# Kernel optimization log

Hardware: AMD Instinct MI355X
Metric: run time of the kernel (lower is better)

## Reference

```python
import jax, jax.numpy as jnp
import numpy as np


def setup_inputs() -> dict:
    key = jax.random.key(0)
    ks = jax.random.split(key, 7)
    Bsz, Dm, L, N = 2, 1536, 2048, 16
    x = jax.random.normal(ks[0], (Bsz, Dm, L), jnp.float32)
    delta = jax.random.uniform(ks[1], (Bsz, Dm, L), jnp.float32, 1e-3, 0.1)  # positive step sizes
    A = -jax.random.uniform(ks[2], (Dm, N), jnp.float32, 0.5, 1.5)  # negative real A for stability
    B = jax.random.normal(ks[3], (Bsz, N, L), jnp.float32)
    C = jax.random.normal(ks[4], (Bsz, N, L), jnp.float32)
    D = jax.random.normal(ks[5], (Dm,), jnp.float32)
    z = jax.random.normal(ks[6], (Bsz, Dm, L), jnp.float32)
    return {"x": x, "delta": delta, "A": A, "B": B, "C": C, "D": D, "z": z}


def reference(x, delta, A, B, C, D, z):
    # x, delta, z: [b, d, l]; A: [d, n]; B, C: [b, n, l]; D: [d]
    dtype_in = x.dtype
    x = x.astype(jnp.float32)
    delta = delta.astype(jnp.float32)
    Bm = B.astype(jnp.float32)
    Cm = C.astype(jnp.float32)

    # time-major for scan: [l, b, ...]
    dl = jnp.moveaxis(delta, 2, 0)   # l b d
    xl = jnp.moveaxis(x, 2, 0)       # l b d
    Bl = jnp.moveaxis(Bm, 2, 0)      # l b n
    Cl = jnp.moveaxis(Cm, 2, 0)      # l b n

    h0 = jnp.zeros((x.shape[0], A.shape[0], A.shape[1]), jnp.float32)  # b d n

    def step(h, inp):
        d_t, x_t, B_t, C_t = inp
        deltaA = jnp.exp(d_t[:, :, None] * A[None, :, :])      # exp(einsum('bdl,dn->bdln')) at token t
        deltaB = d_t[:, :, None] * B_t[:, None, :]              # einsum('bdl,bnl->bdln') at token t
        h = deltaA * h + deltaB * x_t[:, :, None]               # Hx update
        y = jnp.einsum('bdn,bn->bd', h, C_t)                    # Yh readout
        return h, y

    _, ys = jax.lax.scan(step, h0, (dl, xl, Bl, Cl))            # ys: [l, b, d]
    y = jnp.moveaxis(ys, 0, 2)                                  # b d l

    out = y + x * D[None, :, None]
    out = out * jax.nn.silu(z)
    return out.astype(dtype_in)
```

## Files before the change

### kernel.cpp

```cpp
#include <hip/hip_runtime.h>
#include <hip/hip_fp16.h>

#define LOG2E 1.44269504088896340736f
#define DM 1536
#define LL  2048
#define NN  16
#define NCH 64
#define CL  32

__device__ __forceinline__ float fexp2(float v){ return __builtin_amdgcn_exp2f(v); }
__device__ __forceinline__ float frcp(float v){ return __builtin_amdgcn_rcpf(v); }

__device__ __forceinline__ void load16(const float* __restrict__ p, float* v){
    const float4 a=*(const float4*)p,     b=*(const float4*)(p+4),
                 c=*(const float4*)(p+8), d=*(const float4*)(p+12);
    v[0]=a.x; v[1]=a.y; v[2]=a.z; v[3]=a.w;
    v[4]=b.x; v[5]=b.y; v[6]=b.z; v[7]=b.w;
    v[8]=c.x; v[9]=c.y; v[10]=c.z; v[11]=c.w;
    v[12]=d.x; v[13]=d.y; v[14]=d.z; v[15]=d.w;
}

__device__ __forceinline__ float packdx(float d, float x){
    unsigned u = (unsigned)__half_as_ushort(__float2half_rn(d))
               | ((unsigned)__half_as_ushort(__float2half_rn(x)) << 16);
    return __uint_as_float(u);
}
__device__ __forceinline__ void unpackdx(float f, float& d, float& x){
    const unsigned u = __float_as_uint(f);
    d = __half2float(__ushort_as_half((unsigned short)(u & 0xffffu)));
    x = __half2float(__ushort_as_half((unsigned short)(u >> 16)));
}

__global__ __launch_bounds__(256) void transpose_bc(
        const float* __restrict__ Bm, const float* __restrict__ Cm,
        float* __restrict__ Bt, float* __restrict__ Ct){
    const int q  = blockIdx.x*256 + threadIdx.x;
    const int t0 = (q & 511) << 2;
    const int n  = (q >> 9) & 15;
    const int b  = q >> 13;
    const long i = (long)(b*NN + n)*LL + t0;
    const float4 bv = *(const float4*)(Bm + i);
    const float4 cv = *(const float4*)(Cm + i);
    const float bb[4]={bv.x,bv.y,bv.z,bv.w}, cc[4]={cv.x,cv.y,cv.z,cv.w};
#pragma unroll
    for (int j=0;j<4;++j){
        const int t = t0 + j;
        const int o = ((b*CL + (t&31))*NCH + (t>>5))*NN + n;
        Bt[o] = bb[j];
        Ct[o] = cc[j];
    }
}

__global__ __launch_bounds__(256, 3) void ssm_scan(
    const float* __restrict__ x, const float* __restrict__ delta,
    const float* __restrict__ A, const float* __restrict__ Dv,
    const float* __restrict__ z, const float* __restrict__ Bt,
    const float* __restrict__ Ct, float* __restrict__ out)
{
    __shared__ float sdx[4][CL*64];

    const int lane = threadIdx.x & 63;
    const int w    = threadIdx.x >> 6;
    const int row  = blockIdx.x*4 + w;
    const int b    = (row >= DM) ? 1 : 0;
    const int d    = row - b*DM;
    float* sw = sdx[w];

    const long base = (long)row*LL;
    const float* gd = delta + base;
    const float* gx = x + base;

    for (int k=0;k<LL;k+=256){
        const int t0 = k + lane*4;
        const float4 dv = *(const float4*)(gd + t0);
        const float4 xv = *(const float4*)(gx + t0);
        const float dd[4]={dv.x,dv.y,dv.z,dv.w};
        const float xx[4]={xv.x,xv.y,xv.z,xv.w};
#pragma unroll
        for (int j=0;j<4;++j){
            const int t = t0 + j, r = t & 31, c = t >> 5;
            sw[r*64 + (c^r)] = packdx(dd[j], xx[j]);
        }
    }

    float A2[NN];
#pragma unroll
    for (int n=0;n<NN;++n) A2[n] = A[d*NN+n] * LOG2E;

    const float* bq = Bt + (long)b*(CL*NCH*NN) + lane*NN;
    const float* cq = Ct + (long)b*(CL*NCH*NN) + lane*NN;

    float G[NN];
#pragma unroll
    for (int n=0;n<NN;++n) G[n] = 0.f;
    float dsum = 0.f;
    float bb[NN];
    load16(bq, bb);
#pragma unroll 2
    for (int r=0;r<CL;++r){
        float nb[NN];
        if (r+1 < CL) load16(bq + (r+1)*(NCH*NN), nb);
        float d_r, x_r;
        unpackdx(sw[r*64 + (lane^r)], d_r, x_r);
        dsum += d_r;
        const float dx = d_r * x_r;
#pragma unroll
        for (int n=0;n<NN;++n){
            const float e = fexp2(d_r*A2[n]);
            G[n] = __builtin_fmaf(e, G[n], bb[n]*dx);
        }
        if (r+1 < CL){
#pragma unroll
            for (int n=0;n<NN;++n) bb[n] = nb[n];
        }
    }
    float P[NN];
#pragma unroll
    for (int n=0;n<NN;++n) P[n] = fexp2(dsum*A2[n]);

#pragma unroll
    for (int s=1;s<64;s<<=1){
#pragma unroll
        for (int n=0;n<NN;++n){
            const float pl = __shfl_up(P[n], s);
            const float gl = __shfl_up(G[n], s);
            if (lane >= s){
                G[n] = __builtin_fmaf(P[n], gl, G[n]);
                P[n] *= pl;
            }
        }
    }
    float h[NN];
#pragma unroll
    for (int n=0;n<NN;++n){
        const float gp = __shfl_up(G[n], 1);
        h[n] = (lane==0) ? 0.f : gp;
    }

    const float Dd = Dv[d];
    float cc[NN];
    load16(bq, bb);
    load16(cq, cc);
#pragma unroll 2
    for (int r=0;r<CL;++r){
        float nb[NN], nc[NN];
        if (r+1 < CL){
            load16(bq + (r+1)*(NCH*NN), nb);
            load16(cq + (r+1)*(NCH*NN), nc);
        }
        const int a = r*64 + (lane ^ r);
        float d_r, x_r;
        unpackdx(sw[a], d_r, x_r);
        const float dx = d_r * x_r;
        float y0=0.f, y1=0.f, y2=0.f, y3=0.f;
#pragma unroll
        for (int n=0;n<NN;n+=4){
            const float e0=fexp2(d_r*A2[n+0]);
            h[n+0]=__builtin_fmaf(e0,h[n+0],bb[n+0]*dx); y0=__builtin_fmaf(h[n+0],cc[n+0],y0);
            const float e1=fexp2(d_r*A2[n+1]);
            h[n+1]=__builtin_fmaf(e1,h[n+1],bb[n+1]*dx); y1=__builtin_fmaf(h[n+1],cc[n+1],y1);
            const float e2=fexp2(d_r*A2[n+2]);
            h[n+2]=__builtin_fmaf(e2,h[n+2],bb[n+2]*dx); y2=__builtin_fmaf(h[n+2],cc[n+2],y2);
            const float e3=fexp2(d_r*A2[n+3]);
            h[n+3]=__builtin_fmaf(e3,h[n+3],bb[n+3]*dx); y3=__builtin_fmaf(h[n+3],cc[n+3],y3);
        }
        const float y = (y0+y1)+(y2+y3);
        sw[a] = __builtin_fmaf(x_r, Dd, y);
        if (r+1 < CL){
#pragma unroll
            for (int n=0;n<NN;++n){ bb[n]=nb[n]; cc[n]=nc[n]; }
        }
    }

    const float* gz = z + base;
    float* go = out + base;
    for (int k=0;k<LL;k+=256){
        const int t0 = k + lane*4;
        const float4 zv = *(const float4*)(gz + t0);
        const float zz[4]={zv.x,zv.y,zv.z,zv.w};
        float o[4];
#pragma unroll
        for (int j=0;j<4;++j){
            const int t = t0 + j, r = t & 31, c = t >> 5;
            const float yd = sw[r*64 + (c^r)];
            const float sig = frcp(1.f + fexp2(-zz[j]*LOG2E));
            o[j] = yd * (zz[j]*sig);
        }
        float4 o4 = {o[0],o[1],o[2],o[3]};
        *(float4*)(go + t0) = o4;
    }
}

extern "C" void kernel_launch(void* const* d_in, const int* in_sizes, int n_in,
                              void* d_out, int out_size, void* d_ws, size_t ws_size,
                              hipStream_t stream) {
    const float* x     = (const float*)d_in[0];
    const float* delta = (const float*)d_in[1];
    const float* A     = (const float*)d_in[2];
    const float* B     = (const float*)d_in[3];
    const float* C     = (const float*)d_in[4];
    const float* Dv    = (const float*)d_in[5];
    const float* z     = (const float*)d_in[6];
    float* out = (float*)d_out;

    float* Bt = (float*)d_ws;
    float* Ct = Bt + 2*LL*NN;

    transpose_bc<<<dim3(64), dim3(256), 0, stream>>>(B, C, Bt, Ct);
    ssm_scan<<<dim3((2*DM)/4), dim3(256), 0, stream>>>(x, delta, A, Dv, z, Bt, Ct, out);
}
```

Baseline: 185.2 us.

## Process two channels per wavefront and store B/C interleaved in fp16

Each wavefront now scans two d-channels instead of one, so every B/C load serves two channels. B and C are converted to fp16 and interleaved into one 64-byte record per timestep and chunk, which halves their bandwidth and removes the explicit prefetch double-buffering. Blocks shrink to 128 threads with shared memory holding float2 pairs. The trade-offs are higher register pressure from the duplicated 16-element state arrays (launch bounds 128,2) and extra fp16 rounding of B and C.

```diff
diff --git a/kernel.cpp b/kernel.cpp
--- a/kernel.cpp
+++ b/kernel.cpp
@@ -11,15 +11,6 @@
 __device__ __forceinline__ float fexp2(float v){ return __builtin_amdgcn_exp2f(v); }
 __device__ __forceinline__ float frcp(float v){ return __builtin_amdgcn_rcpf(v); }
 
-__device__ __forceinline__ void load16(const float* __restrict__ p, float* v){
-    const float4 a=*(const float4*)p,     b=*(const float4*)(p+4),
-                 c=*(const float4*)(p+8), d=*(const float4*)(p+12);
-    v[0]=a.x; v[1]=a.y; v[2]=a.z; v[3]=a.w;
-    v[4]=b.x; v[5]=b.y; v[6]=b.z; v[7]=b.w;
-    v[8]=c.x; v[9]=c.y; v[10]=c.z; v[11]=c.w;
-    v[12]=d.x; v[13]=d.y; v[14]=d.z; v[15]=d.w;
-}
-
 __device__ __forceinline__ float packdx(float d, float x){
     unsigned u = (unsigned)__half_as_ushort(__float2half_rn(d))
                | ((unsigned)__half_as_ushort(__float2half_rn(x)) << 16);
@@ -30,10 +21,22 @@
     d = __half2float(__ushort_as_half((unsigned short)(u & 0xffffu)));
     x = __half2float(__ushort_as_half((unsigned short)(u >> 16)));
 }
+__device__ __forceinline__ void unpack8(const float4 f, float* o){
+    const unsigned u0=__float_as_uint(f.x), u1=__float_as_uint(f.y),
+                   u2=__float_as_uint(f.z), u3=__float_as_uint(f.w);
+    o[0]=__half2float(__ushort_as_half((unsigned short)(u0&0xffffu)));
+    o[1]=__half2float(__ushort_as_half((unsigned short)(u0>>16)));
+    o[2]=__half2float(__ushort_as_half((unsigned short)(u1&0xffffu)));
+    o[3]=__half2float(__ushort_as_half((unsigned short)(u1>>16)));
+    o[4]=__half2float(__ushort_as_half((unsigned short)(u2&0xffffu)));
+    o[5]=__half2float(__ushort_as_half((unsigned short)(u2>>16)));
+    o[6]=__half2float(__ushort_as_half((unsigned short)(u3&0xffffu)));
+    o[7]=__half2float(__ushort_as_half((unsigned short)(u3>>16)));
+}
 
 __global__ __launch_bounds__(256) void transpose_bc(
         const float* __restrict__ Bm, const float* __restrict__ Cm,
-        float* __restrict__ Bt, float* __restrict__ Ct){
+        __half* __restrict__ BC){
     const int q  = blockIdx.x*256 + threadIdx.x;
     const int t0 = (q & 511) << 2;
     const int n  = (q >> 9) & 15;
@@ -45,149 +48,156 @@
 #pragma unroll
     for (int j=0;j<4;++j){
         const int t = t0 + j;
-        const int o = ((b*CL + (t&31))*NCH + (t>>5))*NN + n;
-        Bt[o] = bb[j];
-        Ct[o] = cc[j];
-    }
-}
-
-__global__ __launch_bounds__(256, 3) void ssm_scan(
+        const long o = ((long)((b*CL + (t&31))*NCH + (t>>5)))*32 + n;
+        BC[o]      = __float2half_rn(bb[j]);
+        BC[o + 16] = __float2half_rn(cc[j]);
+    }
+}
+
+__global__ __launch_bounds__(128, 2) void ssm_scan(
     const float* __restrict__ x, const float* __restrict__ delta,
     const float* __restrict__ A, const float* __restrict__ Dv,
-    const float* __restrict__ z, const float* __restrict__ Bt,
-    const float* __restrict__ Ct, float* __restrict__ out)
+    const float* __restrict__ z, const __half* __restrict__ BC,
+    float* __restrict__ out)
 {
-    __shared__ float sdx[4][CL*64];
+    __shared__ float2 sdx[2][CL*64];
 
     const int lane = threadIdx.x & 63;
     const int w    = threadIdx.x >> 6;
-    const int row  = blockIdx.x*4 + w;
-    const int b    = (row >= DM) ? 1 : 0;
-    const int d    = row - b*DM;
-    float* sw = sdx[w];
-
-    const long base = (long)row*LL;
-    const float* gd = delta + base;
-    const float* gx = x + base;
+    const int row0 = blockIdx.x*4 + w*2;
+    const int b    = (row0 >= DM) ? 1 : 0;
+    const int d0   = row0 - b*DM;
+    float2* sw = sdx[w];
+
+    const long base0 = (long)row0*LL;
+    const long base1 = base0 + LL;
+    const float* gd0 = delta + base0; const float* gx0 = x + base0;
+    const float* gd1 = delta + base1; const float* gx1 = x + base1;
 
     for (int k=0;k<LL;k+=256){
         const int t0 = k + lane*4;
-        const float4 dv = *(const float4*)(gd + t0);
-        const float4 xv = *(const float4*)(gx + t0);
-        const float dd[4]={dv.x,dv.y,dv.z,dv.w};
-        const float xx[4]={xv.x,xv.y,xv.z,xv.w};
+        const float4 dv0 = *(const float4*)(gd0 + t0);
+        const float4 xv0 = *(const float4*)(gx0 + t0);
+        const float4 dv1 = *(const float4*)(gd1 + t0);
+        const float4 xv1 = *(const float4*)(gx1 + t0);
+        const float dd0[4]={dv0.x,dv0.y,dv0.z,dv0.w}, xx0[4]={xv0.x,xv0.y,xv0.z,xv0.w};
+        const float dd1[4]={dv1.x,dv1.y,dv1.z,dv1.w}, xx1[4]={xv1.x,xv1.y,xv1.z,xv1.w};
 #pragma unroll
         for (int j=0;j<4;++j){
             const int t = t0 + j, r = t & 31, c = t >> 5;
-            sw[r*64 + (c^r)] = packdx(dd[j], xx[j]);
-        }
-    }
-
-    float A2[NN];
-#pragma unroll
-    for (int n=0;n<NN;++n) A2[n] = A[d*NN+n] * LOG2E;
-
-    const float* bq = Bt + (long)b*(CL*NCH*NN) + lane*NN;
-    const float* cq = Ct + (long)b*(CL*NCH*NN) + lane*NN;
-
-    float G[NN];
-#pragma unroll
-    for (int n=0;n<NN;++n) G[n] = 0.f;
-    float dsum = 0.f;
-    float bb[NN];
-    load16(bq, bb);
+            float2 wd; wd.x = packdx(dd0[j], xx0[j]); wd.y = packdx(dd1[j], xx1[j]);
+            sw[r*64 + (c^r)] = wd;
+        }
+    }
+
+    float A20[NN], A21[NN];
+#pragma unroll
+    for (int n=0;n<NN;++n){
+        A20[n] = A[d0*NN+n]     * LOG2E;
+        A21[n] = A[(d0+1)*NN+n] * LOG2E;
+    }
+
+    const __half* bc = BC + (long)b*65536 + lane*32;
+
+    float G0[NN], G1[NN];
+#pragma unroll
+    for (int n=0;n<NN;++n){ G0[n]=0.f; G1[n]=0.f; }
+    float ds0=0.f, ds1=0.f;
 #pragma unroll 2
     for (int r=0;r<CL;++r){
-        float nb[NN];
-        if (r+1 < CL) load16(bq + (r+1)*(NCH*NN), nb);
-        float d_r, x_r;
-        unpackdx(sw[r*64 + (lane^r)], d_r, x_r);
-        dsum += d_r;
-        const float dx = d_r * x_r;
+        const float2 wd = sw[r*64 + (lane^r)];
+        const float4* rec = (const float4*)(bc + (long)r*2048);
+        float bb[16];
+        unpack8(rec[0], bb); unpack8(rec[1], bb+8);
+        float d_0,x_0,d_1,x_1;
+        unpackdx(wd.x, d_0, x_0); unpackdx(wd.y, d_1, x_1);
+        ds0 += d_0; ds1 += d_1;
+        const float dx0 = d_0*x_0, dx1 = d_1*x_1;
 #pragma unroll
         for (int n=0;n<NN;++n){
-            const float e = fexp2(d_r*A2[n]);
-            G[n] = __builtin_fmaf(e, G[n], bb[n]*dx);
-        }
-        if (r+1 < CL){
-#pragma unroll
-            for (int n=0;n<NN;++n) bb[n] = nb[n];
-        }
-    }
-    float P[NN];
-#pragma unroll
-    for (int n=0;n<NN;++n) P[n] = fexp2(dsum*A2[n]);
-
-#pragma unroll
-    for (int s=1;s<64;s<<=1){
+            const float e0 = fexp2(d_0*A20[n]);
+            G0[n] = __builtin_fmaf(e0, G0[n], bb[n]*dx0);
+            const float e1 = fexp2(d_1*A21[n]);
+            G1[n] = __builtin_fmaf(e1, G1[n], bb[n]*dx1);
+        }
+    }
+
+    float h0[NN], h1[NN];
+    {
+        float P0[NN], P1[NN];
+#pragma unroll
+        for (int n=0;n<NN;++n){ P0[n]=fexp2(ds0*A20[n]); P1[n]=fexp2(ds1*A21[n]); }
+#pragma unroll
+        for (int s=1;s<64;s<<=1){
+#pragma unroll
+            for (int n=0;n<NN;++n){
+                const float pl0=__shfl_up(P0[n],s), gl0=__shfl_up(G0[n],s);
+                const float pl1=__shfl_up(P1[n],s), gl1=__shfl_up(G1[n],s);
+                if (lane >= s){
+                    G0[n]=__builtin_fmaf(P0[n],gl0,G0[n]); P0[n]*=pl0;
+                    G1[n]=__builtin_fmaf(P1[n],gl1,G1[n]); P1[n]*=pl1;
+                }
+            }
+        }
 #pragma unroll
         for (int n=0;n<NN;++n){
-            const float pl = __shfl_up(P[n], s);
-            const float gl = __shfl_up(G[n], s);
-            if (lane >= s){
-                G[n] = __builtin_fmaf(P[n], gl, G[n]);
-                P[n] *= pl;
-            }
-        }
-    }
-    float h[NN];
-#pragma unroll
-    for (int n=0;n<NN;++n){
-        const float gp = __shfl_up(G[n], 1);
-        h[n] = (lane==0) ? 0.f : gp;
-    }
-
-    const float Dd = Dv[d];
-    float cc[NN];
-    load16(bq, bb);
-    load16(cq, cc);
+            const float g0=__shfl_up(G0[n],1), g1=__shfl_up(G1[n],1);
+            h0[n] = (lane==0)?0.f:g0;
+            h1[n] = (lane==0)?0.f:g1;
+        }
+    }
+
+    const float Dd0 = Dv[d0], Dd1 = Dv[d0+1];
 #pragma unroll 2
     for (int r=0;r<CL;++r){
-        float nb[NN], nc[NN];
-        if (r+1 < CL){
-            load16(bq + (r+1)*(NCH*NN), nb);
-            load16(cq + (r+1)*(NCH*NN), nc);
-        }
-        const int a = r*64 + (lane ^ r);
-        float d_r, x_r;
-        unpackdx(sw[a], d_r, x_r);
-        const float dx = d_r * x_r;
-        float y0=0.f, y1=0.f, y2=0.f, y3=0.f;
-#pragma unroll
-        for (int n=0;n<NN;n+=4){
-            const float e0=fexp2(d_r*A2[n+0]);
-            h[n+0]=__builtin_fmaf(e0,h[n+0],bb[n+0]*dx); y0=__builtin_fmaf(h[n+0],cc[n+0],y0);
-            const float e1=fexp2(d_r*A2[n+1]);
-            h[n+1]=__builtin_fmaf(e1,h[n+1],bb[n+1]*dx); y1=__builtin_fmaf(h[n+1],cc[n+1],y1);
-            const float e2=fexp2(d_r*A2[n+2]);
-            h[n+2]=__builtin_fmaf(e2,h[n+2],bb[n+2]*dx); y2=__builtin_fmaf(h[n+2],cc[n+2],y2);
-            const float e3=fexp2(d_r*A2[n+3]);
-            h[n+3]=__builtin_fmaf(e3,h[n+3],bb[n+3]*dx); y3=__builtin_fmaf(h[n+3],cc[n+3],y3);
-        }
-        const float y = (y0+y1)+(y2+y3);
-        sw[a] = __builtin_fmaf(x_r, Dd, y);
-        if (r+1 < CL){
-#pragma unroll
-            for (int n=0;n<NN;++n){ bb[n]=nb[n]; cc[n]=nc[n]; }
-        }
-    }
-
-    const float* gz = z + base;
-    float* go = out + base;
+        const int slot = r*64 + (lane^r);
+        const float2 wd = sw[slot];
+        const float4* rec = (const float4*)(bc + (long)r*2048);
+        float bb[16], cc[16];
+        unpack8(rec[0], bb); unpack8(rec[1], bb+8);
+        unpack8(rec[2], cc); unpack8(rec[3], cc+8);
+        float d_0,x_0,d_1,x_1;
+        unpackdx(wd.x, d_0, x_0); unpackdx(wd.y, d_1, x_1);
+        const float dx0 = d_0*x_0, dx1 = d_1*x_1;
+        float ya0=0.f, yb0=0.f, ya1=0.f, yb1=0.f;
+#pragma unroll
+        for (int n=0;n<NN;n+=2){
+            const float e0a = fexp2(d_0*A20[n]);
+            h0[n]  =__builtin_fmaf(e0a,h0[n],  bb[n]*dx0);   ya0=__builtin_fmaf(h0[n],  cc[n],  ya0);
+            const float e0b = fexp2(d_0*A20[n+1]);
+            h0[n+1]=__builtin_fmaf(e0b,h0[n+1],bb[n+1]*dx0); yb0=__builtin_fmaf(h0[n+1],cc[n+1],yb0);
+            const float e1a = fexp2(d_1*A21[n]);
+            h1[n]  =__builtin_fmaf(e1a,h1[n],  bb[n]*dx1);   ya1=__builtin_fmaf(h1[n],  cc[n],  ya1);
+            const float e1b = fexp2(d_1*A21[n+1]);
+            h1[n+1]=__builtin_fmaf(e1b,h1[n+1],bb[n+1]*dx1); yb1=__builtin_fmaf(h1[n+1],cc[n+1],yb1);
+        }
+        float2 yo;
+        yo.x = __builtin_fmaf(x_0, Dd0, ya0+yb0);
+        yo.y = __builtin_fmaf(x_1, Dd1, ya1+yb1);
+        sw[slot] = yo;
+    }
+
+    const float* gz0 = z + base0; const float* gz1 = z + base1;
+    float* go0 = out + base0;     float* go1 = out + base1;
     for (int k=0;k<LL;k+=256){
         const int t0 = k + lane*4;
-        const float4 zv = *(const float4*)(gz + t0);
-        const float zz[4]={zv.x,zv.y,zv.z,zv.w};
-        float o[4];
+        const float4 zv0 = *(const float4*)(gz0 + t0);
+        const float4 zv1 = *(const float4*)(gz1 + t0);
+        const float zz0[4]={zv0.x,zv0.y,zv0.z,zv0.w}, zz1[4]={zv1.x,zv1.y,zv1.z,zv1.w};
+        float o0[4], o1[4];
 #pragma unroll
         for (int j=0;j<4;++j){
             const int t = t0 + j, r = t & 31, c = t >> 5;
-            const float yd = sw[r*64 + (c^r)];
-            const float sig = frcp(1.f + fexp2(-zz[j]*LOG2E));
-            o[j] = yd * (zz[j]*sig);
-        }
-        float4 o4 = {o[0],o[1],o[2],o[3]};
-        *(float4*)(go + t0) = o4;
+            const float2 wd = sw[r*64 + (c^r)];
+            const float s0 = frcp(1.f + fexp2(-zz0[j]*LOG2E));
+            const float s1 = frcp(1.f + fexp2(-zz1[j]*LOG2E));
+            o0[j] = wd.x * (zz0[j]*s0);
+            o1[j] = wd.y * (zz1[j]*s1);
+        }
+        float4 a = {o0[0],o0[1],o0[2],o0[3]};
+        float4 bq = {o1[0],o1[1],o1[2],o1[3]};
+        *(float4*)(go0 + t0) = a;
+        *(float4*)(go1 + t0) = bq;
     }
 }
 
@@ -203,9 +213,8 @@
     const float* z     = (const float*)d_in[6];
     float* out = (float*)d_out;
 
-    float* Bt = (float*)d_ws;
-    float* Ct = Bt + 2*LL*NN;
-
-    transpose_bc<<<dim3(64), dim3(256), 0, stream>>>(B, C, Bt, Ct);
-    ssm_scan<<<dim3((2*DM)/4), dim3(256), 0, stream>>>(x, delta, A, Dv, z, Bt, Ct, out);
-}
+    __half* BC = (__half*)d_ws;
+
+    transpose_bc<<<dim3(64), dim3(256), 0, stream>>>(B, C, BC);
+    ssm_scan<<<dim3((2*DM)/4), dim3(128), 0, stream>>>(x, delta, A, Dv, z, BC, out);
+}
```

Result: faster. 167.0 us (-9.8%).
